# Performance work log

Measured on AMD Instinct MI355X. Metric: run time of the kernel, lower is better.

Reference implementation:

```python
import jax, jax.numpy as jnp
import numpy as np

H = 256
H2 = H // 2
N = 1024
T = 12
B = 4


def setup_inputs() -> dict:
    key = jax.random.key(0)
    ks = jax.random.split(key, 12)
    s = lambda fan_in: 1.0 / np.sqrt(fan_in)
    inp = {
        "node_embeddings": jax.random.normal(ks[0], (B, N, H), jnp.float32),
        # origin encoder: Linear(H,H) -> ReLU -> Linear(H,H2)
        "W1o": jax.random.normal(ks[1], (H, H), jnp.float32) * s(H),
        "b1o": jnp.zeros((H,), jnp.float32),
        "W2o": jax.random.normal(ks[2], (H, H2), jnp.float32) * s(H),
        "b2o": jnp.zeros((H2,), jnp.float32),
        # dest encoder
        "W1d": jax.random.normal(ks[3], (H, H), jnp.float32) * s(H),
        "b1d": jnp.zeros((H,), jnp.float32),
        "W2d": jax.random.normal(ks[4], (H, H2), jnp.float32) * s(H),
        "b2d": jnp.zeros((H2,), jnp.float32),
        # bilinear: out = o @ Wb @ d^T + bb  (torch nn.Bilinear(H2,H2,1))
        "Wb": jax.random.normal(ks[5], (H2, H2), jnp.float32) * s(H2),
        "bb": jnp.zeros((), jnp.float32),
        # horizon predictor: Linear(1, T) -> ReLU
        "wh": jax.random.normal(ks[6], (T,), jnp.float32),
        "bh": jnp.zeros((T,), jnp.float32),
    }
    return inp


def reference(node_embeddings, W1o, b1o, W2o, b2o, W1d, b1d, W2d, b2d, Wb, bb, wh, bh):
    # encoders (dropout is identity at eval)
    o = jax.nn.relu(node_embeddings @ W1o + b1o) @ W2o + b2o      # (B,N,H2)
    d = jax.nn.relu(node_embeddings @ W1d + b1d) @ W2d + b2d      # (B,N,H2)
    # bilinear score without materializing (B,N,N,H2):
    oW = jnp.einsum("bik,kl->bil", o, Wb)                          # (B,N,H2)
    scores = jnp.einsum("bil,bjl->bij", oW, d) + bb                # (B,N,N)
    # horizon predictor Linear(1,T)+ReLU, then permute to (B,T,N,N)
    pred = jax.nn.relu(scores[..., None] * wh + bh)                # (B,N,N,T)
    pred = jnp.transpose(pred, (0, 3, 1, 2))                       # (B,T,N,N)
    return jax.nn.relu(pred)
```

## Files before the change

kernel.cpp:

```cpp
#include <hip/hip_runtime.h>

constexpr int H  = 256;
constexpr int H2 = 128;
constexpr int N  = 1024;
constexpr int T  = 12;
constexpr int B  = 4;
constexpr int M  = B * N;

__global__ void fold_wb_kernel(const float* __restrict__ W2o,
                               const float* __restrict__ b2o,
                               const float* __restrict__ Wb,
                               float* __restrict__ W2of,
                               float* __restrict__ b2of) {
    __shared__ float row[H2];
    const int i = blockIdx.x;
    const int j = threadIdx.x;
    const float* src = (i < H) ? (W2o + i * H2) : b2o;
    row[j] = src[j];
    __syncthreads();
    float acc = 0.f;
#pragma unroll 8
    for (int k = 0; k < H2; ++k) acc = fmaf(row[k], Wb[k * H2 + j], acc);
    if (i < H) W2of[i * H2 + j] = acc;
    else       b2of[j] = acc;
}

template<bool RELU, int BK>
__global__ __launch_bounds__(256) void gemm_bias_kernel(
    const float* __restrict__ A0, const float* __restrict__ A1,
    const float* __restrict__ W0, const float* __restrict__ W1,
    const float* __restrict__ bias0, const float* __restrict__ bias1,
    float* __restrict__ C0, float* __restrict__ C1,
    int Nout, int K)
{
    const int br = blockIdx.z;
    const float* A    = br ? A1 : A0;
    const float* W    = br ? W1 : W0;
    const float* bias = br ? bias1 : bias0;
    float*       C    = br ? C1 : C0;

    __shared__ float As[BK][68];
    __shared__ float Ws[BK][68];

    const int tid = threadIdx.x;
    const int tx = tid & 15;
    const int ty = tid >> 4;
    const int row0 = blockIdx.y * 64;
    const int col0 = blockIdx.x * 64;

    float acc[4][4] = {};

    for (int kt = 0; kt < K; kt += BK) {
#pragma unroll
        for (int p = 0; p < (64 * BK / 4) / 256; ++p) {
            const int idx = tid + p * 256;
            const int r  = idx / (BK / 4);
            const int c4 = idx % (BK / 4);
            const float4 v = *(const float4*)(A + (size_t)(row0 + r) * K + kt + 4 * c4);
            As[4 * c4 + 0][r] = v.x;
            As[4 * c4 + 1][r] = v.y;
            As[4 * c4 + 2][r] = v.z;
            As[4 * c4 + 3][r] = v.w;
        }
#pragma unroll
        for (int p = 0; p < (BK * 64 / 4) / 256; ++p) {
            const int idx = tid + p * 256;
            const int r  = idx / 16;
            const int c4 = idx % 16;
            *(float4*)&Ws[r][4 * c4] =
                *(const float4*)(W + (size_t)(kt + r) * Nout + col0 + 4 * c4);
        }
        __syncthreads();
#pragma unroll
        for (int k = 0; k < BK; ++k) {
            const float4 a4 = *(const float4*)&As[k][4 * ty];
            const float4 b4 = *(const float4*)&Ws[k][4 * tx];
            const float a[4] = {a4.x, a4.y, a4.z, a4.w};
            const float b[4] = {b4.x, b4.y, b4.z, b4.w};
#pragma unroll
            for (int i = 0; i < 4; ++i)
#pragma unroll
                for (int j = 0; j < 4; ++j)
                    acc[i][j] = fmaf(a[i], b[j], acc[i][j]);
        }
        __syncthreads();
    }

    const float4 bias4 = *(const float4*)(bias + col0 + 4 * tx);
    const float bj[4] = {bias4.x, bias4.y, bias4.z, bias4.w};
#pragma unroll
    for (int i = 0; i < 4; ++i) {
        float4 o;
        float v0 = acc[i][0] + bj[0];
        float v1 = acc[i][1] + bj[1];
        float v2 = acc[i][2] + bj[2];
        float v3 = acc[i][3] + bj[3];
        if (RELU) {
            v0 = fmaxf(v0, 0.f); v1 = fmaxf(v1, 0.f);
            v2 = fmaxf(v2, 0.f); v3 = fmaxf(v3, 0.f);
        }
        o.x = v0; o.y = v1; o.z = v2; o.w = v3;
        *(float4*)(C + (size_t)(row0 + 4 * ty + i) * Nout + col0 + 4 * tx) = o;
    }
}

template<int BK>
__global__ __launch_bounds__(256) void scores_expand_kernel(
    const float* __restrict__ oW, const float* __restrict__ dd,
    const float* __restrict__ bbp, const float* __restrict__ wh,
    const float* __restrict__ bh, float* __restrict__ out)
{
    __shared__ float As[BK][68];
    __shared__ float Bs[BK][68];
    const int tid = threadIdx.x;
    const int tx = tid & 15;
    const int ty = tid >> 4;
    const int b  = blockIdx.z;
    const int i0 = blockIdx.y * 64;
    const int j0 = blockIdx.x * 64;
    const float* Ab = oW + (size_t)b * N * H2;
    const float* Bb = dd + (size_t)b * N * H2;

    float acc[4][4] = {};

    for (int kt = 0; kt < H2; kt += BK) {
#pragma unroll
        for (int p = 0; p < (64 * BK / 4) / 256; ++p) {
            const int idx = tid + p * 256;
            const int r  = idx / (BK / 4);
            const int c4 = idx % (BK / 4);
            const float4 v = *(const float4*)(Ab + (size_t)(i0 + r) * H2 + kt + 4 * c4);
            As[4 * c4 + 0][r] = v.x;
            As[4 * c4 + 1][r] = v.y;
            As[4 * c4 + 2][r] = v.z;
            As[4 * c4 + 3][r] = v.w;
            const float4 w = *(const float4*)(Bb + (size_t)(j0 + r) * H2 + kt + 4 * c4);
            Bs[4 * c4 + 0][r] = w.x;
            Bs[4 * c4 + 1][r] = w.y;
            Bs[4 * c4 + 2][r] = w.z;
            Bs[4 * c4 + 3][r] = w.w;
        }
        __syncthreads();
#pragma unroll
        for (int k = 0; k < BK; ++k) {
            const float4 a4 = *(const float4*)&As[k][4 * ty];
            const float4 b4 = *(const float4*)&Bs[k][4 * tx];
            const float a[4] = {a4.x, a4.y, a4.z, a4.w};
            const float bfr[4] = {b4.x, b4.y, b4.z, b4.w};
#pragma unroll
            for (int i = 0; i < 4; ++i)
#pragma unroll
                for (int j = 0; j < 4; ++j)
                    acc[i][j] = fmaf(a[i], bfr[j], acc[i][j]);
        }
        __syncthreads();
    }

    const float bbv = bbp[0];
    float whr[T], bhr[T];
#pragma unroll
    for (int t = 0; t < T; ++t) { whr[t] = wh[t]; bhr[t] = bh[t]; }

#pragma unroll
    for (int i = 0; i < 4; ++i)
#pragma unroll
        for (int j = 0; j < 4; ++j)
            acc[i][j] += bbv;

#pragma unroll
    for (int t = 0; t < T; ++t) {
        float* obase = out + ((size_t)(b * T + t) * N + i0 + 4 * ty) * N + j0 + 4 * tx;
#pragma unroll
        for (int i = 0; i < 4; ++i) {
            float4 o;
            o.x = fmaxf(fmaf(acc[i][0], whr[t], bhr[t]), 0.f);
            o.y = fmaxf(fmaf(acc[i][1], whr[t], bhr[t]), 0.f);
            o.z = fmaxf(fmaf(acc[i][2], whr[t], bhr[t]), 0.f);
            o.w = fmaxf(fmaf(acc[i][3], whr[t], bhr[t]), 0.f);
            *(float4*)(obase + (size_t)i * N) = o;
        }
    }
}

extern "C" void kernel_launch(void* const* d_in, const int* in_sizes, int n_in,
                              void* d_out, int out_size, void* d_ws, size_t ws_size,
                              hipStream_t stream) {
    const float* x   = (const float*)d_in[0];
    const float* W1o = (const float*)d_in[1];
    const float* b1o = (const float*)d_in[2];
    const float* W2o = (const float*)d_in[3];
    const float* b2o = (const float*)d_in[4];
    const float* W1d = (const float*)d_in[5];
    const float* b1d = (const float*)d_in[6];
    const float* W2d = (const float*)d_in[7];
    const float* b2d = (const float*)d_in[8];
    const float* Wb  = (const float*)d_in[9];
    const float* bb  = (const float*)d_in[10];
    const float* wh  = (const float*)d_in[11];
    const float* bh  = (const float*)d_in[12];
    float* out = (float*)d_out;

    float* ws   = (float*)d_ws;
    float* W2of = ws;
    float* b2of = W2of + H * H2;
    float* oW   = b2of + H2;
    float* dd   = oW + (size_t)M * H2;
    float* h_o  = dd + (size_t)M * H2;
    float* h_d  = h_o + (size_t)M * H;

    fold_wb_kernel<<<H + 1, H2, 0, stream>>>(W2o, b2o, Wb, W2of, b2of);

    gemm_bias_kernel<true, 32><<<dim3(H / 64, M / 64, 2), 256, 0, stream>>>(
        x, x, W1o, W1d, b1o, b1d, h_o, h_d, H, H);

    gemm_bias_kernel<false, 32><<<dim3(H2 / 64, M / 64, 2), 256, 0, stream>>>(
        h_o, h_d, W2of, W2d, b2of, b2d, oW, dd, H2, H);

    scores_expand_kernel<64><<<dim3(N / 64, N / 64, B), 256, 0, stream>>>(
        oW, dd, bb, wh, bh, out);
}
```

Baseline: 274.5 us.

## Switch encoder and score GEMMs to bf16 MFMA with merged origin/dest weights

Adds a prep kernel that converts the input and the transposed, concatenated weights to bf16. The three GEMM stages are replaced by MFMA 16x16x32 bf16 kernels, and the origin and destination encoders are merged into single wider GEMMs. Intermediates are stored as bf16 to halve traffic, and the score epilogue writes scalar stores in MFMA output layout instead of float4. The aim is to move the compute onto matrix cores. In exchange it gives up fp32 precision, and the 48MB output may now be written with less coalesced scalar stores.

```diff
diff --git a/kernel.cpp b/kernel.cpp
--- a/kernel.cpp
+++ b/kernel.cpp
@@ -1,4 +1,5 @@
 #include <hip/hip_runtime.h>
+#include <hip/hip_bf16.h>
 
 constexpr int H  = 256;
 constexpr int H2 = 128;
@@ -6,6 +7,16 @@
 constexpr int T  = 12;
 constexpr int B  = 4;
 constexpr int M  = B * N;
+
+using short8 = __attribute__((ext_vector_type(8))) short;
+using f32x4  = __attribute__((ext_vector_type(4))) float;
+
+__device__ __forceinline__ unsigned short f2bf(float f) {
+    union { float f; unsigned int u; } v; v.f = f;
+    unsigned int u = v.u;
+    u += 0x7FFFu + ((u >> 16) & 1u);
+    return (unsigned short)(u >> 16);
+}
 
 __global__ void fold_wb_kernel(const float* __restrict__ W2o,
                                const float* __restrict__ b2o,
@@ -25,160 +36,176 @@
     else       b2of[j] = acc;
 }
 
-template<bool RELU, int BK>
-__global__ __launch_bounds__(256) void gemm_bias_kernel(
-    const float* __restrict__ A0, const float* __restrict__ A1,
-    const float* __restrict__ W0, const float* __restrict__ W1,
-    const float* __restrict__ bias0, const float* __restrict__ bias1,
-    float* __restrict__ C0, float* __restrict__ C1,
-    int Nout, int K)
-{
-    const int br = blockIdx.z;
-    const float* A    = br ? A1 : A0;
-    const float* W    = br ? W1 : W0;
-    const float* bias = br ? bias1 : bias0;
-    float*       C    = br ? C1 : C0;
-
-    __shared__ float As[BK][68];
-    __shared__ float Ws[BK][68];
-
+__global__ void prep_kernel(const float* __restrict__ x,
+                            const float* __restrict__ W1o, const float* __restrict__ W1d,
+                            const float* __restrict__ b1o, const float* __restrict__ b1d,
+                            const float* __restrict__ W2of, const float* __restrict__ b2of,
+                            const float* __restrict__ W2d,  const float* __restrict__ b2d,
+                            unsigned short* __restrict__ xb,
+                            unsigned short* __restrict__ W1T,
+                            unsigned short* __restrict__ W2T,
+                            float* __restrict__ bias1, float* __restrict__ bias2)
+{
+    const int NX  = M * H;
+    const int NW1 = 512 * H;
+    const int NW2 = 256 * H;
+    const int TOT = NX + NW1 + NW2 + 512 + 256;
+    for (int i = blockIdx.x * blockDim.x + threadIdx.x; i < TOT;
+         i += gridDim.x * blockDim.x) {
+        if (i < NX) {
+            xb[i] = f2bf(x[i]);
+        } else if (i < NX + NW1) {
+            const int j = i - NX, n = j >> 8, k = j & 255;
+            const float v = (n < 256) ? W1o[k * H + n] : W1d[k * H + (n - 256)];
+            W1T[j] = f2bf(v);
+        } else if (i < NX + NW1 + NW2) {
+            const int j = i - NX - NW1, n = j >> 8, k = j & 255;
+            const float v = (n < 128) ? W2of[k * H2 + n] : W2d[k * H2 + (n - 128)];
+            W2T[j] = f2bf(v);
+        } else if (i < NX + NW1 + NW2 + 512) {
+            const int j = i - NX - NW1 - NW2;
+            bias1[j] = (j < 256) ? b1o[j] : b1d[j - 256];
+        } else {
+            const int j = i - NX - NW1 - NW2 - 512;
+            bias2[j] = (j < 128) ? b2of[j] : b2d[j - 128];
+        }
+    }
+}
+
+template<bool RELU>
+__device__ __forceinline__ void enc_body(
+    const unsigned short* __restrict__ A, int lda,
+    const unsigned short* __restrict__ Bt,
+    const float* __restrict__ bias,
+    unsigned short* __restrict__ C, int ldc)
+{
+    __shared__ unsigned short Abuf[64 * 40];
+    __shared__ unsigned short Bbuf[64 * 40];
     const int tid = threadIdx.x;
-    const int tx = tid & 15;
-    const int ty = tid >> 4;
-    const int row0 = blockIdx.y * 64;
-    const int col0 = blockIdx.x * 64;
-
-    float acc[4][4] = {};
-
-    for (int kt = 0; kt < K; kt += BK) {
-#pragma unroll
-        for (int p = 0; p < (64 * BK / 4) / 256; ++p) {
-            const int idx = tid + p * 256;
-            const int r  = idx / (BK / 4);
-            const int c4 = idx % (BK / 4);
-            const float4 v = *(const float4*)(A + (size_t)(row0 + r) * K + kt + 4 * c4);
-            As[4 * c4 + 0][r] = v.x;
-            As[4 * c4 + 1][r] = v.y;
-            As[4 * c4 + 2][r] = v.z;
-            As[4 * c4 + 3][r] = v.w;
-        }
-#pragma unroll
-        for (int p = 0; p < (BK * 64 / 4) / 256; ++p) {
-            const int idx = tid + p * 256;
-            const int r  = idx / 16;
-            const int c4 = idx % 16;
-            *(float4*)&Ws[r][4 * c4] =
-                *(const float4*)(W + (size_t)(kt + r) * Nout + col0 + 4 * c4);
-        }
+    const int w  = tid >> 6;
+    const int l  = tid & 63;
+    const int lr = tid >> 2;
+    const int lk = (tid & 3) * 8;
+
+    uint4 aR = *(const uint4*)(A + (size_t)lr * lda + lk);
+    uint4 bR = *(const uint4*)(Bt + (size_t)lr * 256 + lk);
+
+    f32x4 z = {0.f, 0.f, 0.f, 0.f};
+    f32x4 acc[4] = {z, z, z, z};
+
+    for (int kc = 0; kc < 256; kc += 32) {
+        if (kc) __syncthreads();
+        *(uint4*)&Abuf[lr * 40 + lk] = aR;
+        *(uint4*)&Bbuf[lr * 40 + lk] = bR;
         __syncthreads();
-#pragma unroll
-        for (int k = 0; k < BK; ++k) {
-            const float4 a4 = *(const float4*)&As[k][4 * ty];
-            const float4 b4 = *(const float4*)&Ws[k][4 * tx];
-            const float a[4] = {a4.x, a4.y, a4.z, a4.w};
-            const float b[4] = {b4.x, b4.y, b4.z, b4.w};
-#pragma unroll
-            for (int i = 0; i < 4; ++i)
-#pragma unroll
-                for (int j = 0; j < 4; ++j)
-                    acc[i][j] = fmaf(a[i], b[j], acc[i][j]);
-        }
-        __syncthreads();
-    }
-
-    const float4 bias4 = *(const float4*)(bias + col0 + 4 * tx);
-    const float bj[4] = {bias4.x, bias4.y, bias4.z, bias4.w};
-#pragma unroll
-    for (int i = 0; i < 4; ++i) {
-        float4 o;
-        float v0 = acc[i][0] + bj[0];
-        float v1 = acc[i][1] + bj[1];
-        float v2 = acc[i][2] + bj[2];
-        float v3 = acc[i][3] + bj[3];
-        if (RELU) {
-            v0 = fmaxf(v0, 0.f); v1 = fmaxf(v1, 0.f);
-            v2 = fmaxf(v2, 0.f); v3 = fmaxf(v3, 0.f);
-        }
-        o.x = v0; o.y = v1; o.z = v2; o.w = v3;
-        *(float4*)(C + (size_t)(row0 + 4 * ty + i) * Nout + col0 + 4 * tx) = o;
-    }
-}
-
-template<int BK>
-__global__ __launch_bounds__(256) void scores_expand_kernel(
-    const float* __restrict__ oW, const float* __restrict__ dd,
+        if (kc + 32 < 256) {
+            aR = *(const uint4*)(A + (size_t)lr * lda + kc + 32 + lk);
+            bR = *(const uint4*)(Bt + (size_t)lr * 256 + kc + 32 + lk);
+        }
+        const int q8 = (l >> 4) * 8;
+        const short8 bf = *(const short8*)&Bbuf[(w * 16 + (l & 15)) * 40 + q8];
+#pragma unroll
+        for (int it = 0; it < 4; ++it) {
+            const short8 af = *(const short8*)&Abuf[(it * 16 + (l & 15)) * 40 + q8];
+            acc[it] = __builtin_amdgcn_mfma_f32_16x16x32_bf16(af, bf, acc[it], 0, 0, 0);
+        }
+    }
+
+    const int n  = w * 16 + (l & 15);
+    const int r0 = (l >> 4) * 4;
+    const float bn = bias[n];
+#pragma unroll
+    for (int it = 0; it < 4; ++it)
+#pragma unroll
+        for (int r = 0; r < 4; ++r) {
+            float v = acc[it][r] + bn;
+            if (RELU) v = fmaxf(v, 0.f);
+            C[(size_t)(it * 16 + r0 + r) * ldc + n] = f2bf(v);
+        }
+}
+
+__global__ __launch_bounds__(256) void enc1_kernel(
+    const unsigned short* __restrict__ xb, const unsigned short* __restrict__ W1T,
+    const float* __restrict__ bias1, unsigned short* __restrict__ h)
+{
+    const int bx = blockIdx.x, by = blockIdx.y;
+    enc_body<true>(xb + (size_t)by * 64 * 256, 256,
+                   W1T + (size_t)bx * 64 * 256,
+                   bias1 + bx * 64,
+                   h + (size_t)by * 64 * 512 + bx * 64, 512);
+}
+
+__global__ __launch_bounds__(256) void enc2_kernel(
+    const unsigned short* __restrict__ h, const unsigned short* __restrict__ W2T,
+    const float* __restrict__ bias2, unsigned short* __restrict__ od)
+{
+    const int bx = blockIdx.x, by = blockIdx.y;
+    enc_body<false>(h + (size_t)by * 64 * 512 + (bx >> 1) * 256, 512,
+                    W2T + (size_t)bx * 64 * 256,
+                    bias2 + bx * 64,
+                    od + (size_t)by * 64 * 256 + bx * 64, 256);
+}
+
+__global__ __launch_bounds__(256) void k3_kernel(
+    const unsigned short* __restrict__ od,
     const float* __restrict__ bbp, const float* __restrict__ wh,
     const float* __restrict__ bh, float* __restrict__ out)
 {
-    __shared__ float As[BK][68];
-    __shared__ float Bs[BK][68];
+    __shared__ unsigned short Abuf[64 * 40];
+    __shared__ unsigned short Bbuf[64 * 40];
     const int tid = threadIdx.x;
-    const int tx = tid & 15;
-    const int ty = tid >> 4;
+    const int w  = tid >> 6;
+    const int l  = tid & 63;
+    const int lr = tid >> 2;
+    const int lk = (tid & 3) * 8;
     const int b  = blockIdx.z;
     const int i0 = blockIdx.y * 64;
     const int j0 = blockIdx.x * 64;
-    const float* Ab = oW + (size_t)b * N * H2;
-    const float* Bb = dd + (size_t)b * N * H2;
-
-    float acc[4][4] = {};
-
-    for (int kt = 0; kt < H2; kt += BK) {
-#pragma unroll
-        for (int p = 0; p < (64 * BK / 4) / 256; ++p) {
-            const int idx = tid + p * 256;
-            const int r  = idx / (BK / 4);
-            const int c4 = idx % (BK / 4);
-            const float4 v = *(const float4*)(Ab + (size_t)(i0 + r) * H2 + kt + 4 * c4);
-            As[4 * c4 + 0][r] = v.x;
-            As[4 * c4 + 1][r] = v.y;
-            As[4 * c4 + 2][r] = v.z;
-            As[4 * c4 + 3][r] = v.w;
-            const float4 w = *(const float4*)(Bb + (size_t)(j0 + r) * H2 + kt + 4 * c4);
-            Bs[4 * c4 + 0][r] = w.x;
-            Bs[4 * c4 + 1][r] = w.y;
-            Bs[4 * c4 + 2][r] = w.z;
-            Bs[4 * c4 + 3][r] = w.w;
-        }
+    const unsigned short* Ab = od + ((size_t)b * N + i0) * 256;
+    const unsigned short* Bb = od + ((size_t)b * N + j0) * 256 + 128;
+
+    uint4 aR = *(const uint4*)(Ab + (size_t)lr * 256 + lk);
+    uint4 bR = *(const uint4*)(Bb + (size_t)lr * 256 + lk);
+
+    f32x4 z = {0.f, 0.f, 0.f, 0.f};
+    f32x4 acc[4] = {z, z, z, z};
+
+    for (int kc = 0; kc < H2; kc += 32) {
+        if (kc) __syncthreads();
+        *(uint4*)&Abuf[lr * 40 + lk] = aR;
+        *(uint4*)&Bbuf[lr * 40 + lk] = bR;
         __syncthreads();
-#pragma unroll
-        for (int k = 0; k < BK; ++k) {
-            const float4 a4 = *(const float4*)&As[k][4 * ty];
-            const float4 b4 = *(const float4*)&Bs[k][4 * tx];
-            const float a[4] = {a4.x, a4.y, a4.z, a4.w};
-            const float bfr[4] = {b4.x, b4.y, b4.z, b4.w};
-#pragma unroll
-            for (int i = 0; i < 4; ++i)
-#pragma unroll
-                for (int j = 0; j < 4; ++j)
-                    acc[i][j] = fmaf(a[i], bfr[j], acc[i][j]);
-        }
-        __syncthreads();
+        if (kc + 32 < H2) {
+            aR = *(const uint4*)(Ab + (size_t)lr * 256 + kc + 32 + lk);
+            bR = *(const uint4*)(Bb + (size_t)lr * 256 + kc + 32 + lk);
+        }
+        const int q8 = (l >> 4) * 8;
+        const short8 bf = *(const short8*)&Bbuf[(w * 16 + (l & 15)) * 40 + q8];
+#pragma unroll
+        for (int it = 0; it < 4; ++it) {
+            const short8 af = *(const short8*)&Abuf[(it * 16 + (l & 15)) * 40 + q8];
+            acc[it] = __builtin_amdgcn_mfma_f32_16x16x32_bf16(af, bf, acc[it], 0, 0, 0);
+        }
     }
 
     const float bbv = bbp[0];
-    float whr[T], bhr[T];
-#pragma unroll
-    for (int t = 0; t < T; ++t) { whr[t] = wh[t]; bhr[t] = bh[t]; }
-
-#pragma unroll
-    for (int i = 0; i < 4; ++i)
-#pragma unroll
-        for (int j = 0; j < 4; ++j)
-            acc[i][j] += bbv;
-
+    float s[4][4];
+#pragma unroll
+    for (int it = 0; it < 4; ++it)
+#pragma unroll
+        for (int r = 0; r < 4; ++r) s[it][r] = acc[it][r] + bbv;
+
+    const int jcol = j0 + w * 16 + (l & 15);
+    const int r0   = (l >> 4) * 4;
 #pragma unroll
     for (int t = 0; t < T; ++t) {
-        float* obase = out + ((size_t)(b * T + t) * N + i0 + 4 * ty) * N + j0 + 4 * tx;
-#pragma unroll
-        for (int i = 0; i < 4; ++i) {
-            float4 o;
-            o.x = fmaxf(fmaf(acc[i][0], whr[t], bhr[t]), 0.f);
-            o.y = fmaxf(fmaf(acc[i][1], whr[t], bhr[t]), 0.f);
-            o.z = fmaxf(fmaf(acc[i][2], whr[t], bhr[t]), 0.f);
-            o.w = fmaxf(fmaf(acc[i][3], whr[t], bhr[t]), 0.f);
-            *(float4*)(obase + (size_t)i * N) = o;
-        }
+        const float wt = wh[t], bt = bh[t];
+        float* ob = out + ((size_t)(b * T + t) * N + i0 + r0) * N + jcol;
+#pragma unroll
+        for (int it = 0; it < 4; ++it)
+#pragma unroll
+            for (int r = 0; r < 4; ++r)
+                ob[(size_t)(it * 16 + r) * N] = fmaxf(fmaf(s[it][r], wt, bt), 0.f);
     }
 }
 
@@ -200,22 +227,25 @@
     const float* bh  = (const float*)d_in[12];
     float* out = (float*)d_out;
 
-    float* ws   = (float*)d_ws;
-    float* W2of = ws;
-    float* b2of = W2of + H * H2;
-    float* oW   = b2of + H2;
-    float* dd   = oW + (size_t)M * H2;
-    float* h_o  = dd + (size_t)M * H2;
-    float* h_d  = h_o + (size_t)M * H;
+    float* W2of  = (float*)d_ws;
+    float* b2of  = W2of + H * H2;
+    float* bias1 = b2of + H2;
+    float* bias2 = bias1 + 512;
+    unsigned short* xb  = (unsigned short*)(bias2 + 256);
+    unsigned short* W1T = xb + (size_t)M * H;
+    unsigned short* W2T = W1T + 512 * H;
+    unsigned short* h   = W2T + 256 * H;
+    unsigned short* od  = h + (size_t)M * 512;
 
     fold_wb_kernel<<<H + 1, H2, 0, stream>>>(W2o, b2o, Wb, W2of, b2of);
 
-    gemm_bias_kernel<true, 32><<<dim3(H / 64, M / 64, 2), 256, 0, stream>>>(
-        x, x, W1o, W1d, b1o, b1d, h_o, h_d, H, H);
-
-    gemm_bias_kernel<false, 32><<<dim3(H2 / 64, M / 64, 2), 256, 0, stream>>>(
-        h_o, h_d, W2of, W2d, b2of, b2d, oW, dd, H2, H);
-
-    scores_expand_kernel<64><<<dim3(N / 64, N / 64, B), 256, 0, stream>>>(
-        oW, dd, bb, wh, bh, out);
-}
+    prep_kernel<<<1024, 256, 0, stream>>>(x, W1o, W1d, b1o, b1d,
+                                          W2of, b2of, W2d, b2d,
+                                          xb, W1T, W2T, bias1, bias2);
+
+    enc1_kernel<<<dim3(8, M / 64), 256, 0, stream>>>(xb, W1T, bias1, h);
+
+    enc2_kernel<<<dim3(4, M / 64), 256, 0, stream>>>(h, W2T, bias2, od);
+
+    k3_kernel<<<dim3(N / 64, N / 64, B), 256, 0, stream>>>(od, bb, wh, bh, out);
+}
```

Result: faster. 250.7 us (-8.7%).
